# Optimization experiments

Hardware: AMD Instinct MI355X
Metric: run time of the kernel (lower is better)

Reference implementation:

```python
import jax, jax.numpy as jnp
import numpy as np

B, L, D, H, WIN, EXP = 2, 4096, 1024, 16, 256, 4

def setup_inputs() -> dict:
    key = jax.random.key(0)
    ks = jax.random.split(key, 8)
    F = EXP * D
    p = lambda k, shape: jax.random.normal(k, shape, dtype=jnp.float32) * 0.02
    return {
        "x": jax.random.normal(ks[0], (B, L, D), dtype=jnp.float32),
        "mask": jnp.zeros((B, L), dtype=jnp.float32),  # 0 = local attention everywhere
        "Wq": p(ks[1], (D, D)), "bq": jnp.zeros((D,), jnp.float32),
        "Wk": p(ks[2], (D, D)), "bk": jnp.zeros((D,), jnp.float32),
        "Wv": p(ks[3], (D, D)), "bv": jnp.zeros((D,), jnp.float32),
        "ln_g": jnp.ones((D,), jnp.float32), "ln_b": jnp.zeros((D,), jnp.float32),
        "W1": p(ks[4], (D, F)), "b1": jnp.zeros((F,), jnp.float32),
        "W2": p(ks[5], (F, D)), "b2": jnp.zeros((D,), jnp.float32),
    }


def reference(x, mask, Wq, bq, Wk, bk, Wv, bv, ln_g, ln_b, W1, b1, W2, b2):
    NEG = jnp.asarray(-1e9, x.dtype)
    Bs, Ls, Ds = x.shape
    dh = Ds // H
    c = WIN // 2  # one-sided window size (HF uses attention_window // 2)
    pad = WIN - Ls % WIN
    xp = jnp.pad(x, ((0, 0), (0, pad), (0, 0)))  # pad_token_id == 0
    mp = jnp.pad(mask, ((0, 0), (0, pad)), constant_values=-10000.0)
    S = Ls + pad
    n = S // c  # number of query chunks of size c

    inv_sqrt_dh = jnp.asarray(1.0 / np.sqrt(dh), x.dtype)
    q = ((xp @ Wq + bq) * inv_sqrt_dh).reshape(Bs, S, H, dh)
    k = (xp @ Wk + bk).reshape(Bs, S, H, dh)
    v = (xp @ Wv + bv).reshape(Bs, S, H, dh)

    # pad keys/values by one chunk on each side so query chunk i sees chunks i-1,i,i+1
    kp = jnp.pad(k, ((0, 0), (c, c), (0, 0), (0, 0)))
    vp = jnp.pad(v, ((0, 0), (c, c), (0, 0), (0, 0)))
    kvalid = jnp.pad(mp == 0.0, ((0, 0), (c, c)), constant_values=False)  # [B, S+2c]

    idx = jnp.arange(n)[:, None] * c + jnp.arange(3 * c)[None, :]  # [n, 3c]
    kc = kp[:, idx]   # [B, n, 3c, H, dh]
    vc = vp[:, idx]   # [B, n, 3c, H, dh]
    kvc = kvalid[:, idx]  # [B, n, 3c]
    qc = q.reshape(Bs, n, c, H, dh)

    scores = jnp.einsum('bnphd,bnrhd->bhnpr', qc, kc)  # [B,H,n,c,3c]
    p_ = jnp.arange(c)[:, None]
    r_ = jnp.arange(3 * c)[None, :]
    band = (r_ >= p_) & (r_ <= p_ + 2 * c)  # exact |i-j| <= c band, [c,3c]
    valid = band[None, None, None, :, :] & kvc[:, None, :, None, :]
    scores = jnp.where(valid, scores, NEG)
    probs = jax.nn.softmax(scores, axis=-1)
    attn = jnp.einsum('bhnpr,bnrhd->bnphd', probs, vc).reshape(Bs, S, Ds)

    h = (xp + attn)[:, :Ls]  # residual then drop padding (matches module order)
    mu = jnp.mean(h, axis=-1, keepdims=True)
    var = jnp.var(h, axis=-1, keepdims=True)
    h = (h - mu) / jnp.sqrt(var + 1e-5) * ln_g + ln_b
    out = h + (jax.nn.gelu(h @ W1 + b1, approximate=False) @ W2 + b2)
    return out
```

## Files before the change

### kernel.cpp

```cpp
#include <hip/hip_runtime.h>
#include <hip/hip_bf16.h>
#include <cstdint>

typedef __attribute__((ext_vector_type(8))) short short8;
typedef __attribute__((ext_vector_type(4))) short short4v;
typedef __attribute__((ext_vector_type(4))) float floatx4;

constexpr int B_ = 2, L_ = 4096, D_ = 1024, H_ = 16, DH = 64, F_ = 4096;
constexpr int M_ = B_ * L_;
constexpr int NQKV = 3 * D_;
constexpr int VT_GUARD = 512;

constexpr size_t OFF_XB  = 0;
constexpr size_t OFF_WCT = OFF_XB  + (size_t)M_ * D_ * 2;
constexpr size_t OFF_W1T = OFF_WCT + (size_t)NQKV * D_ * 2;
constexpr size_t OFF_W2T = OFF_W1T + (size_t)F_ * D_ * 2;
constexpr size_t OFF_QKV = OFF_W2T + (size_t)D_ * F_ * 2;
constexpr size_t OFF_VT  = OFF_QKV + (size_t)M_ * NQKV * 2;
constexpr size_t OFF_ATT = OFF_VT  + ((size_t)B_*H_*DH*L_ + 2*VT_GUARD) * 2;
constexpr size_t OFF_HB  = OFF_ATT + (size_t)M_ * D_ * 2;
constexpr size_t OFF_MID = OFF_HB  + (size_t)M_ * D_ * 2;

static __device__ __forceinline__ float b2f(unsigned short u) {
    union { unsigned int i; float f; } v; v.i = ((unsigned int)u) << 16; return v.f;
}

static __device__ __forceinline__ void gload16(const void* g, void* l) {
    __builtin_amdgcn_global_load_lds(
        (const __attribute__((address_space(1))) uint32_t*)g,
        (__attribute__((address_space(3))) uint32_t*)l, 16, 0, 0);
}

__global__ __launch_bounds__(256) void k_cvt_x(const float* __restrict__ x,
                                               __hip_bfloat16* __restrict__ xb) {
    int i = (blockIdx.x * 256 + threadIdx.x) * 8;
    float4 a = *(const float4*)(x + i);
    float4 b = *(const float4*)(x + i + 4);
    alignas(16) __hip_bfloat16 t[8];
    t[0] = __float2bfloat16(a.x); t[1] = __float2bfloat16(a.y);
    t[2] = __float2bfloat16(a.z); t[3] = __float2bfloat16(a.w);
    t[4] = __float2bfloat16(b.x); t[5] = __float2bfloat16(b.y);
    t[6] = __float2bfloat16(b.z); t[7] = __float2bfloat16(b.w);
    *(uint4*)(xb + i) = *(const uint4*)t;
}

__global__ __launch_bounds__(256) void k_tcvt(const float* __restrict__ in,
                                              __hip_bfloat16* __restrict__ out,
                                              int R, int C) {
    __shared__ float t[64][65];
    int tx = threadIdx.x & 63, ty4 = threadIdx.x >> 6;
    int c0 = blockIdx.x * 64, r0 = blockIdx.y * 64;
#pragma unroll
    for (int i = 0; i < 16; i++) {
        int r = ty4 + i * 4;
        t[r][tx] = in[(size_t)(r0 + r) * C + c0 + tx];
    }
    __syncthreads();
#pragma unroll
    for (int i = 0; i < 16; i++) {
        int r = ty4 + i * 4;
        out[(size_t)(c0 + r) * R + r0 + tx] = __float2bfloat16(t[tx][r]);
    }
}

__global__ __launch_bounds__(256) void k_vtrans(const __hip_bfloat16* __restrict__ qkv,
                                                __hip_bfloat16* __restrict__ vtg) {
    __shared__ __hip_bfloat16 t[64][72];
    int tx = threadIdx.x & 63, ty4 = threadIdx.x >> 6;
    int bh = blockIdx.y, b = bh >> 4, h = bh & 15;
    int j0 = blockIdx.x * 64;
#pragma unroll
    for (int i = 0; i < 16; i++) {
        int j = ty4 + i * 4;
        t[j][tx] = qkv[(size_t)(b * L_ + j0 + j) * NQKV + 2 * D_ + h * DH + tx];
    }
    __syncthreads();
#pragma unroll
    for (int i = 0; i < 16; i++) {
        int d = ty4 + i * 4;
        vtg[(long)(bh * DH + d) * L_ + j0 + tx] = t[tx][d];
    }
}

template<int EPI>
__global__ __launch_bounds__(256, 2)
void k_gemm(const __hip_bfloat16* __restrict__ A, const __hip_bfloat16* __restrict__ BT,
            int M, int N, int K,
            const float* __restrict__ bias0, const float* __restrict__ bias1,
            const float* __restrict__ bias2,
            __hip_bfloat16* __restrict__ obf, float* __restrict__ of32,
            const __hip_bfloat16* __restrict__ hres) {
    __shared__ __hip_bfloat16 As[128 * 64];
    __shared__ __hip_bfloat16 Bs[128 * 64];
    const int tid = threadIdx.x, wave = tid >> 6, lane = tid & 63;
    const int m0 = blockIdx.x * 128, n0 = blockIdx.y * 128;
    const int wr = wave >> 1, wc = wave & 1;
    const int lo = lane & 15, hi = lane >> 4;
    floatx4 acc[4][4] = {};

    for (int kt = 0; kt < K; kt += 64) {
        __syncthreads();
#pragma unroll
        for (int i = 0; i < 4; i++) {
            int chunk = i * 256 + tid;
            const __hip_bfloat16* ga = A + (size_t)(m0 + (chunk >> 3)) * K + kt + (chunk & 7) * 8;
            gload16(ga, As + (size_t)(i * 256 + wave * 64) * 8);
            const __hip_bfloat16* gb = BT + (size_t)(n0 + (chunk >> 3)) * K + kt + (chunk & 7) * 8;
            gload16(gb, Bs + (size_t)(i * 256 + wave * 64) * 8);
        }
        __syncthreads();
#pragma unroll
        for (int kk = 0; kk < 2; kk++) {
            short8 af[4], bf[4];
#pragma unroll
            for (int mt = 0; mt < 4; mt++)
                af[mt] = *(const short8*)(As + (wr * 64 + mt * 16 + lo) * 64 + kk * 32 + hi * 8);
#pragma unroll
            for (int nt = 0; nt < 4; nt++)
                bf[nt] = *(const short8*)(Bs + (wc * 64 + nt * 16 + lo) * 64 + kk * 32 + hi * 8);
#pragma unroll
            for (int mt = 0; mt < 4; mt++)
#pragma unroll
                for (int nt = 0; nt < 4; nt++)
                    acc[mt][nt] = __builtin_amdgcn_mfma_f32_16x16x32_bf16(af[mt], bf[nt], acc[mt][nt], 0, 0, 0);
        }
    }

#pragma unroll
    for (int mt = 0; mt < 4; mt++) {
#pragma unroll
        for (int nt = 0; nt < 4; nt++) {
            int col = n0 + wc * 64 + nt * 16 + lo;
#pragma unroll
            for (int r = 0; r < 4; r++) {
                int row = m0 + wr * 64 + mt * 16 + hi * 4 + r;
                float v = acc[mt][nt][r];
                if (EPI == 0) {
                    float bia = (col < 1024) ? bias0[col]
                              : (col < 2048 ? bias1[col - 1024] : bias2[col - 2048]);
                    obf[(size_t)row * NQKV + col] = __float2bfloat16(v + bia);
                } else if (EPI == 1) {
                    v += bias0[col];
                    v = 0.5f * v * (1.0f + erff(v * 0.70710678118654752440f));
                    obf[(size_t)row * F_ + col] = __float2bfloat16(v);
                } else {
                    v += bias0[col];
                    v += b2f(*(const unsigned short*)&hres[(size_t)row * D_ + col]);
                    of32[(size_t)row * D_ + col] = v;
                }
            }
        }
    }
}

__global__ __launch_bounds__(256, 2)
void k_attn(const __hip_bfloat16* __restrict__ qkv, const float* __restrict__ mask,
            const __hip_bfloat16* __restrict__ vtg, __hip_bfloat16* __restrict__ attnb) {
    constexpr int PS = 296;
    __shared__ __hip_bfloat16 P[4][16 * PS];
    const int tid = threadIdx.x, wave = tid >> 6, lane = tid & 63;
    const int bh = blockIdx.y, b = bh >> 4, h = bh & 15;
    const int q0 = blockIdx.x * 64 + wave * 16;
    const int lo = lane & 15, hi = lane >> 4;

    short8 qf0, qf1;
    {
        const __hip_bfloat16* qb = qkv + (size_t)(b * L_ + q0 + lo) * NQKV + h * DH + hi * 8;
        qf0 = *(const short8*)qb;
        qf1 = *(const short8*)(qb + 32);
    }

    floatx4 sc[17];
    const __hip_bfloat16* kcol = qkv + (size_t)b * L_ * NQKV + D_ + h * DH + hi * 8;
#pragma unroll
    for (int t = 0; t < 17; t++) {
        int jg = q0 - 128 + t * 16 + lo;
        int jc = jg < 0 ? 0 : (jg >= L_ ? L_ - 1 : jg);
        const __hip_bfloat16* kb = kcol + (size_t)jc * NQKV;
        short8 kf0 = *(const short8*)kb;
        short8 kf1 = *(const short8*)(kb + 32);
        floatx4 a = {};
        a = __builtin_amdgcn_mfma_f32_16x16x32_bf16(qf0, kf0, a, 0, 0, 0);
        a = __builtin_amdgcn_mfma_f32_16x16x32_bf16(qf1, kf1, a, 0, 0, 0);
        float mval = mask[b * L_ + jc];
        bool jok = (jg >= 0) && (jg < L_) && (mval == 0.0f);
#pragma unroll
        for (int r = 0; r < 4; r++) {
            int qi = q0 + hi * 4 + r;
            bool ok = jok && (jg >= qi - 128) && (jg <= qi + 128);
            a[r] = ok ? a[r] * 0.125f : -1e9f;
        }
        sc[t] = a;
    }

#pragma unroll
    for (int r = 0; r < 4; r++) {
        float m = -3e38f;
#pragma unroll
        for (int t = 0; t < 17; t++) m = fmaxf(m, sc[t][r]);
        m = fmaxf(m, __shfl_xor(m, 1));
        m = fmaxf(m, __shfl_xor(m, 2));
        m = fmaxf(m, __shfl_xor(m, 4));
        m = fmaxf(m, __shfl_xor(m, 8));
        float s = 0.0f;
#pragma unroll
        for (int t = 0; t < 17; t++) { float e = __expf(sc[t][r] - m); sc[t][r] = e; s += e; }
        s += __shfl_xor(s, 1); s += __shfl_xor(s, 2);
        s += __shfl_xor(s, 4); s += __shfl_xor(s, 8);
        float inv = 1.0f / s;
#pragma unroll
        for (int t = 0; t < 17; t++) sc[t][r] *= inv;
    }

    __hip_bfloat16* Pw = &P[wave][0];
#pragma unroll
    for (int t = 0; t < 17; t++)
#pragma unroll
        for (int r = 0; r < 4; r++)
            Pw[(hi * 4 + r) * PS + t * 16 + lo] = __float2bfloat16(sc[t][r]);
    {
        int zr = lane >> 2, zc = 272 + (lane & 3) * 4;
        __hip_bfloat16 z = __float2bfloat16(0.0f);
#pragma unroll
        for (int i = 0; i < 4; i++) Pw[zr * PS + zc + i] = z;
    }

    floatx4 o[4] = {};
#pragma unroll
    for (int st = 0; st < 9; st++) {
        short8 pa = *(const short8*)(Pw + lo * PS + st * 32 + hi * 8);
        int jb = q0 - 128 + st * 32 + hi * 8;
#pragma unroll
        for (int dt = 0; dt < 4; dt++) {
            const __hip_bfloat16* vb = vtg + (long)(bh * DH + dt * 16 + lo) * L_ + jb;
            short8 vf = *(const short8*)vb;
            o[dt] = __builtin_amdgcn_mfma_f32_16x16x32_bf16(pa, vf, o[dt], 0, 0, 0);
        }
    }

#pragma unroll
    for (int dt = 0; dt < 4; dt++)
#pragma unroll
        for (int r = 0; r < 4; r++) {
            int row = q0 + hi * 4 + r;
            attnb[(size_t)(b * L_ + row) * D_ + h * DH + dt * 16 + lo] =
                __float2bfloat16(o[dt][r]);
        }
}

__global__ __launch_bounds__(256)
void k_ln(const float* __restrict__ x, const __hip_bfloat16* __restrict__ attnb,
          const float* __restrict__ g, const float* __restrict__ bt,
          __hip_bfloat16* __restrict__ hb) {
    const int row = blockIdx.x, tid = threadIdx.x;
    const int c4 = tid * 4;
    float4 xv = *(const float4*)(x + (size_t)row * D_ + c4);
    short4v av = *(const short4v*)(attnb + (size_t)row * D_ + c4);
    float h0 = xv.x + b2f((unsigned short)av[0]);
    float h1 = xv.y + b2f((unsigned short)av[1]);
    float h2 = xv.z + b2f((unsigned short)av[2]);
    float h3 = xv.w + b2f((unsigned short)av[3]);
    float s = h0 + h1 + h2 + h3;
    float q = h0 * h0 + h1 * h1 + h2 * h2 + h3 * h3;
#pragma unroll
    for (int off = 32; off > 0; off >>= 1) {
        s += __shfl_down(s, off);
        q += __shfl_down(q, off);
    }
    __shared__ float red[8];
    int wave = tid >> 6, lane = tid & 63;
    if (lane == 0) { red[wave] = s; red[4 + wave] = q; }
    __syncthreads();
    s = red[0] + red[1] + red[2] + red[3];
    q = red[4] + red[5] + red[6] + red[7];
    float mu = s * (1.0f / D_);
    float var = q * (1.0f / D_) - mu * mu;
    float inv = rsqrtf(var + 1e-5f);
    float4 gv = *(const float4*)(g + c4);
    float4 bv = *(const float4*)(bt + c4);
    alignas(8) __hip_bfloat16 ov[4];
    ov[0] = __float2bfloat16((h0 - mu) * inv * gv.x + bv.x);
    ov[1] = __float2bfloat16((h1 - mu) * inv * gv.y + bv.y);
    ov[2] = __float2bfloat16((h2 - mu) * inv * gv.z + bv.z);
    ov[3] = __float2bfloat16((h3 - mu) * inv * gv.w + bv.w);
    *(short4v*)(hb + (size_t)row * D_ + c4) = *(const short4v*)ov;
}

extern "C" void kernel_launch(void* const* d_in, const int* in_sizes, int n_in,
                              void* d_out, int out_size, void* d_ws, size_t ws_size,
                              hipStream_t stream) {
    const float* x    = (const float*)d_in[0];
    const float* mask = (const float*)d_in[1];
    const float* Wq   = (const float*)d_in[2];
    const float* bq   = (const float*)d_in[3];
    const float* Wk   = (const float*)d_in[4];
    const float* bk   = (const float*)d_in[5];
    const float* Wv   = (const float*)d_in[6];
    const float* bv   = (const float*)d_in[7];
    const float* ln_g = (const float*)d_in[8];
    const float* ln_b = (const float*)d_in[9];
    const float* W1   = (const float*)d_in[10];
    const float* b1   = (const float*)d_in[11];
    const float* W2   = (const float*)d_in[12];
    const float* b2   = (const float*)d_in[13];
    float* out = (float*)d_out;
    char* ws = (char*)d_ws;

    __hip_bfloat16* xb   = (__hip_bfloat16*)(ws + OFF_XB);
    __hip_bfloat16* wct  = (__hip_bfloat16*)(ws + OFF_WCT);
    __hip_bfloat16* w1t  = (__hip_bfloat16*)(ws + OFF_W1T);
    __hip_bfloat16* w2t  = (__hip_bfloat16*)(ws + OFF_W2T);
    __hip_bfloat16* qkvb = (__hip_bfloat16*)(ws + OFF_QKV);
    __hip_bfloat16* vtg  = (__hip_bfloat16*)(ws + OFF_VT) + VT_GUARD;
    __hip_bfloat16* attb = (__hip_bfloat16*)(ws + OFF_ATT);
    __hip_bfloat16* hb   = (__hip_bfloat16*)(ws + OFF_HB);
    __hip_bfloat16* midb = (__hip_bfloat16*)(ws + OFF_MID);

    k_cvt_x<<<(M_ * D_) / 2048, 256, 0, stream>>>(x, xb);
    k_tcvt<<<dim3(D_ / 64, D_ / 64), 256, 0, stream>>>(Wq, wct,                 D_, D_);
    k_tcvt<<<dim3(D_ / 64, D_ / 64), 256, 0, stream>>>(Wk, wct + 1024 * 1024,   D_, D_);
    k_tcvt<<<dim3(D_ / 64, D_ / 64), 256, 0, stream>>>(Wv, wct + 2 * 1024 * 1024, D_, D_);
    k_tcvt<<<dim3(F_ / 64, D_ / 64), 256, 0, stream>>>(W1, w1t, D_, F_);
    k_tcvt<<<dim3(D_ / 64, F_ / 64), 256, 0, stream>>>(W2, w2t, F_, D_);

    k_gemm<0><<<dim3(M_ / 128, NQKV / 128), 256, 0, stream>>>(
        xb, wct, M_, NQKV, D_, bq, bk, bv, qkvb, nullptr, nullptr);

    k_vtrans<<<dim3(L_ / 64, B_ * H_), 256, 0, stream>>>(qkvb, vtg);
    k_attn<<<dim3(L_ / 64, B_ * H_), 256, 0, stream>>>(qkvb, mask, vtg, attb);

    k_ln<<<M_, 256, 0, stream>>>(x, attb, ln_g, ln_b, hb);

    k_gemm<1><<<dim3(M_ / 128, F_ / 128), 256, 0, stream>>>(
        hb, w1t, M_, F_, D_, b1, nullptr, nullptr, midb, nullptr, nullptr);
    k_gemm<2><<<dim3(M_ / 128, D_ / 128), 256, 0, stream>>>(
        midb, w2t, M_, D_, F_, b2, nullptr, nullptr, nullptr, out, hb);
}
```

Baseline: 503.5 us.

## Replace GEMM with 8-wave 256-row double-buffered pipelined kernel

Replaces the 128x128, 4-wave GEMM with an 8-wave kernel that computes 256xBN tiles. It double-buffers LDS in two K-halves, issues global-to-LDS loads for the next tile while MFMAs run, and uses explicit barriers, waitcnt and setprio. It also adds an XOR swizzle to LDS to avoid bank conflicts and a workgroup ID remap for L2 locality. The aim is to hide memory latency and raise MFMA utilisation in the three large GEMMs, at the cost of hand-tuned synchronisation and high register pressure from the 8xNF accumulators.

New measurement: 539.6 us. 1.07x slower.

```diff
diff --git a/kernel.cpp b/kernel.cpp
--- a/kernel.cpp
+++ b/kernel.cpp
@@ -29,6 +29,21 @@
     __builtin_amdgcn_global_load_lds(
         (const __attribute__((address_space(1))) uint32_t*)g,
         (__attribute__((address_space(3))) uint32_t*)l, 16, 0, 0);
+}
+
+static __device__ __forceinline__ void bar() {
+    asm volatile("" ::: "memory");
+    __builtin_amdgcn_s_barrier();
+    asm volatile("" ::: "memory");
+}
+static __device__ __forceinline__ void waitlgk0() {
+    asm volatile("s_waitcnt lgkmcnt(0)" ::: "memory");
+    __builtin_amdgcn_sched_barrier(0);
+}
+template<int N> static __device__ __forceinline__ void waitvm() {
+    if constexpr (N == 3)      asm volatile("s_waitcnt vmcnt(3)" ::: "memory");
+    else if constexpr (N == 4) asm volatile("s_waitcnt vmcnt(4)" ::: "memory");
+    else                       asm volatile("s_waitcnt vmcnt(0)" ::: "memory");
 }
 
 __global__ __launch_bounds__(256) void k_cvt_x(const float* __restrict__ x,
@@ -82,71 +97,150 @@
     }
 }
 
-template<int EPI>
-__global__ __launch_bounds__(256, 2)
-void k_gemm(const __hip_bfloat16* __restrict__ A, const __hip_bfloat16* __restrict__ BT,
-            int M, int N, int K,
-            const float* __restrict__ bias0, const float* __restrict__ bias1,
-            const float* __restrict__ bias2,
-            __hip_bfloat16* __restrict__ obf, float* __restrict__ of32,
-            const __hip_bfloat16* __restrict__ hres) {
-    __shared__ __hip_bfloat16 As[128 * 64];
-    __shared__ __hip_bfloat16 Bs[128 * 64];
+template<int NF, int EPI, int NTOT, int KTOT>
+__global__ __launch_bounds__(512, 2)
+void k_gemm8(const __hip_bfloat16* __restrict__ A, const __hip_bfloat16* __restrict__ BT,
+             const float* __restrict__ b0p, const float* __restrict__ b1p,
+             const float* __restrict__ b2p,
+             __hip_bfloat16* __restrict__ obf, float* __restrict__ of32,
+             const __hip_bfloat16* __restrict__ hres) {
+    constexpr int BN = NF * 64;
+    constexpr int BLOADS = NF / 2;
+    constexpr int UU = 2 + BLOADS;
+    constexpr int KT = KTOT / 64;
+    constexpr int MB = 32;
+
+    __shared__ __hip_bfloat16 As[2][2][256 * 32];
+    __shared__ __hip_bfloat16 Bs[2][2][BN * 32];
+
     const int tid = threadIdx.x, wave = tid >> 6, lane = tid & 63;
-    const int m0 = blockIdx.x * 128, n0 = blockIdx.y * 128;
-    const int wr = wave >> 1, wc = wave & 1;
     const int lo = lane & 15, hi = lane >> 4;
-    floatx4 acc[4][4] = {};
-
-    for (int kt = 0; kt < K; kt += 64) {
-        __syncthreads();
-#pragma unroll
-        for (int i = 0; i < 4; i++) {
-            int chunk = i * 256 + tid;
-            const __hip_bfloat16* ga = A + (size_t)(m0 + (chunk >> 3)) * K + kt + (chunk & 7) * 8;
-            gload16(ga, As + (size_t)(i * 256 + wave * 64) * 8);
-            const __hip_bfloat16* gb = BT + (size_t)(n0 + (chunk >> 3)) * K + kt + (chunk & 7) * 8;
-            gload16(gb, Bs + (size_t)(i * 256 + wave * 64) * 8);
-        }
-        __syncthreads();
-#pragma unroll
-        for (int kk = 0; kk < 2; kk++) {
-            short8 af[4], bf[4];
-#pragma unroll
-            for (int mt = 0; mt < 4; mt++)
-                af[mt] = *(const short8*)(As + (wr * 64 + mt * 16 + lo) * 64 + kk * 32 + hi * 8);
-#pragma unroll
-            for (int nt = 0; nt < 4; nt++)
-                bf[nt] = *(const short8*)(Bs + (wc * 64 + nt * 16 + lo) * 64 + kk * 32 + hi * 8);
-#pragma unroll
-            for (int mt = 0; mt < 4; mt++)
-#pragma unroll
-                for (int nt = 0; nt < 4; nt++)
-                    acc[mt][nt] = __builtin_amdgcn_mfma_f32_16x16x32_bf16(af[mt], bf[nt], acc[mt][nt], 0, 0, 0);
-        }
-    }
-
-#pragma unroll
-    for (int mt = 0; mt < 4; mt++) {
-#pragma unroll
-        for (int nt = 0; nt < 4; nt++) {
-            int col = n0 + wc * 64 + nt * 16 + lo;
-#pragma unroll
-            for (int r = 0; r < 4; r++) {
-                int row = m0 + wr * 64 + mt * 16 + hi * 4 + r;
-                float v = acc[mt][nt][r];
+    const int wm = wave >> 2, wn = wave & 3;
+
+    const int nwg = gridDim.x, q = nwg >> 3;
+    const int bid = blockIdx.x;
+    const int swz = (bid & 7) * q + (bid >> 3);
+    const int bm = swz & (MB - 1), bn = swz >> 5;
+    const size_t m0 = (size_t)bm * 256, n0 = (size_t)bn * BN;
+
+    const int rowT = tid >> 2;
+    const int chunkT = (((tid & 3) ^ ((tid >> 3) & 3))) * 8;
+    const __hip_bfloat16* aG = A  + (m0 + rowT) * (size_t)KTOT + chunkT;
+    const __hip_bfloat16* bG = BT + (n0 + rowT) * (size_t)KTOT + chunkT;
+
+    const int swz16 = (hi ^ ((lo >> 1) & 3)) * 8;
+    const int aOff = (wm * 128 + lo) * 32 + swz16;
+    const int bOff = (wn * (NF * 16) + lo) * 32 + swz16;
+
+    floatx4 acc[8][NF] = {};
+
+#define STAGE_A(nb2, kh, kcol)                                              \
+    _Pragma("unroll")                                                       \
+    for (int s = 0; s < 2; ++s)                                             \
+        gload16(aG + (size_t)s * 128 * KTOT + (kcol),                       \
+                &As[nb2][kh][(s * 512 + wave * 64) * 8]);
+#define STAGE_B(nb2, kh, kcol)                                              \
+    _Pragma("unroll")                                                       \
+    for (int s = 0; s < BLOADS; ++s)                                        \
+        gload16(bG + (size_t)s * 128 * KTOT + (kcol),                       \
+                &Bs[nb2][kh][(s * 512 + wave * 64) * 8]);
+
+    STAGE_A(0, 0, 0); STAGE_B(0, 0, 0);
+    STAGE_A(0, 1, 32); STAGE_B(0, 1, 32);
+    waitvm<UU>();
+    bar();
+
+#pragma unroll 2
+    for (int kt = 0; kt < KT; ++kt) {
+        const int cur = kt & 1, nxt = cur ^ 1;
+        const int kn = ((kt + 1 < KT) ? (kt + 1) : kt) * 64;
+        short8 bfr[NF], afr[4];
+        const __hip_bfloat16* aL0 = &As[cur][0][0];
+        const __hip_bfloat16* bL0 = &Bs[cur][0][0];
+        const __hip_bfloat16* aL1 = &As[cur][1][0];
+        const __hip_bfloat16* bL1 = &Bs[cur][1][0];
+
+#pragma unroll
+        for (int nf = 0; nf < NF; ++nf) bfr[nf] = *(const short8*)(bL0 + bOff + nf * 512);
+#pragma unroll
+        for (int mf = 0; mf < 4; ++mf) afr[mf] = *(const short8*)(aL0 + aOff + mf * 512);
+        STAGE_A(nxt, 0, kn); STAGE_B(nxt, 0, kn);
+        bar(); waitlgk0();
+        __builtin_amdgcn_s_setprio(1);
+#pragma unroll
+        for (int mf = 0; mf < 4; ++mf)
+#pragma unroll
+            for (int nf = 0; nf < NF; ++nf)
+                acc[mf][nf] = __builtin_amdgcn_mfma_f32_16x16x32_bf16(afr[mf], bfr[nf], acc[mf][nf], 0, 0, 0);
+        __builtin_amdgcn_s_setprio(0);
+        bar();
+
+#pragma unroll
+        for (int mf = 0; mf < 4; ++mf) afr[mf] = *(const short8*)(aL0 + aOff + (4 + mf) * 512);
+        bar(); waitlgk0();
+        __builtin_amdgcn_s_setprio(1);
+#pragma unroll
+        for (int mf = 0; mf < 4; ++mf)
+#pragma unroll
+            for (int nf = 0; nf < NF; ++nf)
+                acc[4 + mf][nf] = __builtin_amdgcn_mfma_f32_16x16x32_bf16(afr[mf], bfr[nf], acc[4 + mf][nf], 0, 0, 0);
+        __builtin_amdgcn_s_setprio(0);
+        waitvm<UU>();
+        bar();
+
+#pragma unroll
+        for (int nf = 0; nf < NF; ++nf) bfr[nf] = *(const short8*)(bL1 + bOff + nf * 512);
+#pragma unroll
+        for (int mf = 0; mf < 4; ++mf) afr[mf] = *(const short8*)(aL1 + aOff + mf * 512);
+        STAGE_A(nxt, 1, kn + 32); STAGE_B(nxt, 1, kn + 32);
+        bar(); waitlgk0();
+        __builtin_amdgcn_s_setprio(1);
+#pragma unroll
+        for (int mf = 0; mf < 4; ++mf)
+#pragma unroll
+            for (int nf = 0; nf < NF; ++nf)
+                acc[mf][nf] = __builtin_amdgcn_mfma_f32_16x16x32_bf16(afr[mf], bfr[nf], acc[mf][nf], 0, 0, 0);
+        __builtin_amdgcn_s_setprio(0);
+        bar();
+
+#pragma unroll
+        for (int mf = 0; mf < 4; ++mf) afr[mf] = *(const short8*)(aL1 + aOff + (4 + mf) * 512);
+        bar(); waitlgk0();
+        __builtin_amdgcn_s_setprio(1);
+#pragma unroll
+        for (int mf = 0; mf < 4; ++mf)
+#pragma unroll
+            for (int nf = 0; nf < NF; ++nf)
+                acc[4 + mf][nf] = __builtin_amdgcn_mfma_f32_16x16x32_bf16(afr[mf], bfr[nf], acc[4 + mf][nf], 0, 0, 0);
+        __builtin_amdgcn_s_setprio(0);
+        waitvm<UU>();
+        bar();
+    }
+#undef STAGE_A
+#undef STAGE_B
+
+#pragma unroll
+    for (int mf = 0; mf < 8; ++mf) {
+        const int row = (int)m0 + wm * 128 + mf * 16 + hi * 4;
+#pragma unroll
+        for (int nf = 0; nf < NF; ++nf) {
+            const int col = (int)n0 + wn * (NF * 16) + nf * 16 + lo;
+#pragma unroll
+            for (int r = 0; r < 4; ++r) {
+                float v = acc[mf][nf][r];
+                const size_t ro = (size_t)(row + r);
                 if (EPI == 0) {
-                    float bia = (col < 1024) ? bias0[col]
-                              : (col < 2048 ? bias1[col - 1024] : bias2[col - 2048]);
-                    obf[(size_t)row * NQKV + col] = __float2bfloat16(v + bia);
+                    float bia = (col < 1024) ? b0p[col]
+                              : (col < 2048 ? b1p[col - 1024] : b2p[col - 2048]);
+                    obf[ro * NQKV + col] = __float2bfloat16(v + bia);
                 } else if (EPI == 1) {
-                    v += bias0[col];
+                    v += b0p[col];
                     v = 0.5f * v * (1.0f + erff(v * 0.70710678118654752440f));
-                    obf[(size_t)row * F_ + col] = __float2bfloat16(v);
+                    obf[ro * F_ + col] = __float2bfloat16(v);
                 } else {
-                    v += bias0[col];
-                    v += b2f(*(const unsigned short*)&hres[(size_t)row * D_ + col]);
-                    of32[(size_t)row * D_ + col] = v;
+                    v += b0p[col];
+                    v += b2f(*(const unsigned short*)&hres[ro * D_ + col]);
+                    of32[ro * D_ + col] = v;
                 }
             }
         }
@@ -317,22 +411,22 @@
     __hip_bfloat16* midb = (__hip_bfloat16*)(ws + OFF_MID);
 
     k_cvt_x<<<(M_ * D_) / 2048, 256, 0, stream>>>(x, xb);
-    k_tcvt<<<dim3(D_ / 64, D_ / 64), 256, 0, stream>>>(Wq, wct,                 D_, D_);
-    k_tcvt<<<dim3(D_ / 64, D_ / 64), 256, 0, stream>>>(Wk, wct + 1024 * 1024,   D_, D_);
+    k_tcvt<<<dim3(D_ / 64, D_ / 64), 256, 0, stream>>>(Wq, wct,                   D_, D_);
+    k_tcvt<<<dim3(D_ / 64, D_ / 64), 256, 0, stream>>>(Wk, wct + 1024 * 1024,     D_, D_);
     k_tcvt<<<dim3(D_ / 64, D_ / 64), 256, 0, stream>>>(Wv, wct + 2 * 1024 * 1024, D_, D_);
     k_tcvt<<<dim3(F_ / 64, D_ / 64), 256, 0, stream>>>(W1, w1t, D_, F_);
     k_tcvt<<<dim3(D_ / 64, F_ / 64), 256, 0, stream>>>(W2, w2t, F_, D_);
 
-    k_gemm<0><<<dim3(M_ / 128, NQKV / 128), 256, 0, stream>>>(
-        xb, wct, M_, NQKV, D_, bq, bk, bv, qkvb, nullptr, nullptr);
+    k_gemm8<4, 0, NQKV, D_><<<32 * (NQKV / 256), 512, 0, stream>>>(
+        xb, wct, bq, bk, bv, qkvb, nullptr, nullptr);
 
     k_vtrans<<<dim3(L_ / 64, B_ * H_), 256, 0, stream>>>(qkvb, vtg);
     k_attn<<<dim3(L_ / 64, B_ * H_), 256, 0, stream>>>(qkvb, mask, vtg, attb);
 
     k_ln<<<M_, 256, 0, stream>>>(x, attb, ln_g, ln_b, hb);
 
-    k_gemm<1><<<dim3(M_ / 128, F_ / 128), 256, 0, stream>>>(
-        hb, w1t, M_, F_, D_, b1, nullptr, nullptr, midb, nullptr, nullptr);
-    k_gemm<2><<<dim3(M_ / 128, D_ / 128), 256, 0, stream>>>(
-        midb, w2t, M_, D_, F_, b2, nullptr, nullptr, nullptr, out, hb);
-}
+    k_gemm8<4, 1, F_, D_><<<32 * (F_ / 256), 512, 0, stream>>>(
+        hb, w1t, b1, nullptr, nullptr, midb, nullptr, nullptr);
+    k_gemm8<2, 2, D_, F_><<<32 * (D_ / 128), 512, 0, stream>>>(
+        midb, w2t, b2, nullptr, nullptr, nullptr, out, hb);
+}
```

## Rewrite GEMM with double-buffered LDS, swizzled layout and grouped tile scheduling

Applied to the files above, without the earlier changes.

Replaces the generic GEMM with a templated kernel that prefetches the next K-tile into a second LDS buffer while the current tile runs MFMAs. The kernel needs only one barrier per iteration instead of two. LDS is split into 32-wide K halves with an XOR swizzle to cut bank conflicts, and block IDs are remapped into grouped M-tiles (with an XCD-style interleave) to improve L2 reuse. This doubles LDS use (64KB per block), which may limit occupancy to one block per CU despite the launch bounds.

New measurement: 549.5 us. +9.1%, slower.

```diff
diff --git a/kernel.cpp b/kernel.cpp
--- a/kernel.cpp
+++ b/kernel.cpp
@@ -82,75 +82,117 @@
     }
 }
 
-template<int EPI>
+template<int NBN, int GM, int EPI, int KTOT>
 __global__ __launch_bounds__(256, 2)
-void k_gemm(const __hip_bfloat16* __restrict__ A, const __hip_bfloat16* __restrict__ BT,
-            int M, int N, int K,
-            const float* __restrict__ bias0, const float* __restrict__ bias1,
-            const float* __restrict__ bias2,
-            __hip_bfloat16* __restrict__ obf, float* __restrict__ of32,
-            const __hip_bfloat16* __restrict__ hres) {
-    __shared__ __hip_bfloat16 As[128 * 64];
-    __shared__ __hip_bfloat16 Bs[128 * 64];
+void k_g2(const __hip_bfloat16* __restrict__ A, const __hip_bfloat16* __restrict__ BT,
+          const float* __restrict__ b0p, const float* __restrict__ b1p,
+          const float* __restrict__ b2p,
+          __hip_bfloat16* __restrict__ obf, float* __restrict__ of32,
+          const __hip_bfloat16* __restrict__ hres) {
+    constexpr int KT = KTOT / 64;
+    constexpr int NTOT = NBN * 128;
+    constexpr int PER = GM * NBN;
+    __shared__ __hip_bfloat16 As[2 * 2 * 128 * 32];
+    __shared__ __hip_bfloat16 Bs[2 * 2 * 128 * 32];
+
     const int tid = threadIdx.x, wave = tid >> 6, lane = tid & 63;
-    const int m0 = blockIdx.x * 128, n0 = blockIdx.y * 128;
-    const int wr = wave >> 1, wc = wave & 1;
     const int lo = lane & 15, hi = lane >> 4;
+    const int wm = wave >> 1, wn = wave & 1;
+
+    const int nwg = gridDim.x, q = nwg >> 3;
+    const int bid = blockIdx.x;
+    const int swz = (bid & 7) * q + (bid >> 3);
+    const int g = swz / PER, r = swz % PER;
+    const int bm = g * GM + (r % GM);
+    const int bn = r / GM;
+    const size_t m0 = (size_t)bm * 128, n0 = (size_t)bn * 128;
+
+    const int chunkT = ((tid & 3) ^ ((tid >> 3) & 3)) * 8;
+    const __hip_bfloat16* aG = A  + (m0 + (tid >> 2)) * (size_t)KTOT + chunkT;
+    const __hip_bfloat16* bG = BT + (n0 + (tid >> 2)) * (size_t)KTOT + chunkT;
+    const int ldsOff = wave * 512;
+
+    const int swz16 = (hi ^ ((lo >> 1) & 3)) * 8;
+    const int aOff = (wm * 64 + lo) * 32 + swz16;
+    const int bOff = (wn * 64 + lo) * 32 + swz16;
+
     floatx4 acc[4][4] = {};
 
-    for (int kt = 0; kt < K; kt += 64) {
-        __syncthreads();
-#pragma unroll
-        for (int i = 0; i < 4; i++) {
-            int chunk = i * 256 + tid;
-            const __hip_bfloat16* ga = A + (size_t)(m0 + (chunk >> 3)) * K + kt + (chunk & 7) * 8;
-            gload16(ga, As + (size_t)(i * 256 + wave * 64) * 8);
-            const __hip_bfloat16* gb = BT + (size_t)(n0 + (chunk >> 3)) * K + kt + (chunk & 7) * 8;
-            gload16(gb, Bs + (size_t)(i * 256 + wave * 64) * 8);
-        }
-        __syncthreads();
-#pragma unroll
-        for (int kk = 0; kk < 2; kk++) {
-            short8 af[4], bf[4];
-#pragma unroll
-            for (int mt = 0; mt < 4; mt++)
-                af[mt] = *(const short8*)(As + (wr * 64 + mt * 16 + lo) * 64 + kk * 32 + hi * 8);
-#pragma unroll
-            for (int nt = 0; nt < 4; nt++)
-                bf[nt] = *(const short8*)(Bs + (wc * 64 + nt * 16 + lo) * 64 + kk * 32 + hi * 8);
-#pragma unroll
-            for (int mt = 0; mt < 4; mt++)
-#pragma unroll
-                for (int nt = 0; nt < 4; nt++)
-                    acc[mt][nt] = __builtin_amdgcn_mfma_f32_16x16x32_bf16(af[mt], bf[nt], acc[mt][nt], 0, 0, 0);
-        }
-    }
-
-#pragma unroll
-    for (int mt = 0; mt < 4; mt++) {
-#pragma unroll
-        for (int nt = 0; nt < 4; nt++) {
-            int col = n0 + wc * 64 + nt * 16 + lo;
-#pragma unroll
-            for (int r = 0; r < 4; r++) {
-                int row = m0 + wr * 64 + mt * 16 + hi * 4 + r;
-                float v = acc[mt][nt][r];
+#define STAGE(buf, t)                                                         \
+    _Pragma("unroll")                                                         \
+    for (int kh = 0; kh < 2; ++kh)                                            \
+        _Pragma("unroll")                                                     \
+        for (int s = 0; s < 2; ++s) {                                         \
+            gload16(aG + (size_t)(t) * 64 + kh * 32 + (size_t)s * 64 * KTOT,  \
+                    As + (buf * 2 + kh) * 4096 + s * 2048 + ldsOff);          \
+            gload16(bG + (size_t)(t) * 64 + kh * 32 + (size_t)s * 64 * KTOT,  \
+                    Bs + (buf * 2 + kh) * 4096 + s * 2048 + ldsOff);          \
+        }
+
+    STAGE(0, 0)
+    asm volatile("s_waitcnt vmcnt(0)" ::: "memory");
+    __builtin_amdgcn_s_barrier();
+
+    for (int t = 0; t < KT; ++t) {
+        const int cur = t & 1;
+        if (t + 1 < KT) {
+            const int nxt = cur ^ 1;
+            STAGE(nxt, t + 1)
+        }
+        const __hip_bfloat16* aU0 = As + (cur * 2 + 0) * 4096;
+        const __hip_bfloat16* bU0 = Bs + (cur * 2 + 0) * 4096;
+        const __hip_bfloat16* aU1 = As + (cur * 2 + 1) * 4096;
+        const __hip_bfloat16* bU1 = Bs + (cur * 2 + 1) * 4096;
+#pragma unroll
+        for (int kh = 0; kh < 2; ++kh) {
+            const __hip_bfloat16* aU = kh ? aU1 : aU0;
+            const __hip_bfloat16* bU = kh ? bU1 : bU0;
+            short8 afr[4], bfr[4];
+#pragma unroll
+            for (int i = 0; i < 4; ++i) {
+                afr[i] = *(const short8*)(aU + aOff + i * 512);
+                bfr[i] = *(const short8*)(bU + bOff + i * 512);
+            }
+#pragma unroll
+            for (int mf = 0; mf < 4; ++mf)
+#pragma unroll
+                for (int nf = 0; nf < 4; ++nf)
+                    acc[mf][nf] = __builtin_amdgcn_mfma_f32_16x16x32_bf16(
+                        afr[mf], bfr[nf], acc[mf][nf], 0, 0, 0);
+        }
+        asm volatile("s_waitcnt vmcnt(0)" ::: "memory");
+        __builtin_amdgcn_sched_barrier(0);
+        __builtin_amdgcn_s_barrier();
+    }
+#undef STAGE
+
+#pragma unroll
+    for (int mf = 0; mf < 4; ++mf) {
+        const int row = (int)m0 + wm * 64 + mf * 16 + hi * 4;
+#pragma unroll
+        for (int nf = 0; nf < 4; ++nf) {
+            const int col = (int)n0 + wn * 64 + nf * 16 + lo;
+#pragma unroll
+            for (int rr = 0; rr < 4; ++rr) {
+                float v = acc[mf][nf][rr];
+                const size_t ro = (size_t)(row + rr);
                 if (EPI == 0) {
-                    float bia = (col < 1024) ? bias0[col]
-                              : (col < 2048 ? bias1[col - 1024] : bias2[col - 2048]);
-                    obf[(size_t)row * NQKV + col] = __float2bfloat16(v + bia);
+                    float bia = (col < 1024) ? b0p[col]
+                              : (col < 2048 ? b1p[col - 1024] : b2p[col - 2048]);
+                    obf[ro * NQKV + col] = __float2bfloat16(v + bia);
                 } else if (EPI == 1) {
-                    v += bias0[col];
+                    v += b0p[col];
                     v = 0.5f * v * (1.0f + erff(v * 0.70710678118654752440f));
-                    obf[(size_t)row * F_ + col] = __float2bfloat16(v);
+                    obf[ro * F_ + col] = __float2bfloat16(v);
                 } else {
-                    v += bias0[col];
-                    v += b2f(*(const unsigned short*)&hres[(size_t)row * D_ + col]);
-                    of32[(size_t)row * D_ + col] = v;
+                    v += b0p[col];
+                    v += b2f(*(const unsigned short*)&hres[ro * D_ + col]);
+                    of32[ro * D_ + col] = v;
                 }
             }
         }
     }
+    (void)NTOT;
 }
 
 __global__ __launch_bounds__(256, 2)
@@ -317,22 +359,22 @@
     __hip_bfloat16* midb = (__hip_bfloat16*)(ws + OFF_MID);
 
     k_cvt_x<<<(M_ * D_) / 2048, 256, 0, stream>>>(x, xb);
-    k_tcvt<<<dim3(D_ / 64, D_ / 64), 256, 0, stream>>>(Wq, wct,                 D_, D_);
-    k_tcvt<<<dim3(D_ / 64, D_ / 64), 256, 0, stream>>>(Wk, wct + 1024 * 1024,   D_, D_);
+    k_tcvt<<<dim3(D_ / 64, D_ / 64), 256, 0, stream>>>(Wq, wct,                   D_, D_);
+    k_tcvt<<<dim3(D_ / 64, D_ / 64), 256, 0, stream>>>(Wk, wct + 1024 * 1024,     D_, D_);
     k_tcvt<<<dim3(D_ / 64, D_ / 64), 256, 0, stream>>>(Wv, wct + 2 * 1024 * 1024, D_, D_);
     k_tcvt<<<dim3(F_ / 64, D_ / 64), 256, 0, stream>>>(W1, w1t, D_, F_);
     k_tcvt<<<dim3(D_ / 64, F_ / 64), 256, 0, stream>>>(W2, w2t, F_, D_);
 
-    k_gemm<0><<<dim3(M_ / 128, NQKV / 128), 256, 0, stream>>>(
-        xb, wct, M_, NQKV, D_, bq, bk, bv, qkvb, nullptr, nullptr);
+    k_g2<24, 8, 0, D_><<<64 * 24, 256, 0, stream>>>(
+        xb, wct, bq, bk, bv, qkvb, nullptr, nullptr);
 
     k_vtrans<<<dim3(L_ / 64, B_ * H_), 256, 0, stream>>>(qkvb, vtg);
     k_attn<<<dim3(L_ / 64, B_ * H_), 256, 0, stream>>>(qkvb, mask, vtg, attb);
 
     k_ln<<<M_, 256, 0, stream>>>(x, attb, ln_g, ln_b, hb);
 
-    k_gemm<1><<<dim3(M_ / 128, F_ / 128), 256, 0, stream>>>(
-        hb, w1t, M_, F_, D_, b1, nullptr, nullptr, midb, nullptr, nullptr);
-    k_gemm<2><<<dim3(M_ / 128, D_ / 128), 256, 0, stream>>>(
-        midb, w2t, M_, D_, F_, b2, nullptr, nullptr, nullptr, out, hb);
-}
+    k_g2<32, 8, 1, D_><<<64 * 32, 256, 0, stream>>>(
+        hb, w1t, b1, nullptr, nullptr, midb, nullptr, nullptr);
+    k_g2<8, 2, 2, F_><<<64 * 8, 256, 0, stream>>>(
+        midb, w2t, b2, nullptr, nullptr, nullptr, out, hb);
+}
```
